# Kernel optimization log

Hardware: AMD Instinct MI355X
Metric: run time of the kernel (lower is better)

The kernel has to match this reference:

```python
import jax, jax.numpy as jnp
import numpy as np


def setup_inputs() -> dict:
    key = jax.random.key(0)
    k_x, k_q, k_k, k_v = jax.random.split(key, 4)
    B, C, H, W = 4, 256, 64, 64
    Cq = C // 4
    scale = 0.02
    x = jax.random.normal(k_x, (B, C, H, W), dtype=jnp.float32)
    Wq = jax.random.normal(k_q, (C, Cq), dtype=jnp.float32) * scale
    Wk = jax.random.normal(k_k, (C, Cq), dtype=jnp.float32) * scale
    Wv = jax.random.normal(k_v, (C, C), dtype=jnp.float32) * scale
    gamma = jnp.array([0.5], dtype=jnp.float32)
    return {"x": x, "Wq": Wq, "Wk": Wk, "Wv": Wv, "gamma": gamma}


def reference(x, Wq, Wk, Wv, gamma):
    B, C, H, W = x.shape
    N = H * W
    # [B,C,H,W] -> [B, N, C]
    xf = x.transpose(0, 2, 3, 1).reshape(B, N, C)
    q = jnp.einsum('bnc,cd->bnd', xf, Wq)   # [B, N, C//4]
    k = jnp.einsum('bnc,cd->bnd', xf, Wk)   # [B, N, C//4]
    v = jnp.einsum('bnc,cd->bnd', xf, Wv)   # [B, N, C]
    scores = jnp.einsum('bqd,bkd->bqk', q, k)        # [B, Nq, Nk]
    # NOTE: softmax over the QUERY axis (dim=1), matching the torch module.
    attn = jax.nn.softmax(scores, axis=1)
    out = gamma * jnp.einsum('bqk,bkc->bqc', attn, v) + xf   # [B, N, C]
    # [B, N, C] -> [B, C, N] -> [B, C, H, W]
    return out.transpose(0, 2, 1).reshape(B, C, H, W)
```

## Files before the change

### kernel.cpp

```cpp
#include <hip/hip_runtime.h>
#include <hip/hip_bf16.h>

#define B_ 4
#define C_ 256
#define N_ 4096
#define Dh 64

typedef __attribute__((ext_vector_type(8))) short short8;
typedef __attribute__((ext_vector_type(4))) float f32x4;


__device__ __forceinline__ ushort f2bf(float f) {
    union { float f; unsigned u; } v; v.f = f;
    unsigned u = v.u;
    return (ushort)((u + 0x7fffu + ((u >> 16) & 1u)) >> 16);
}

__device__ __forceinline__ unsigned pack2_bf16(float lo, float hi) {
    const unsigned ulo = __float_as_uint(lo) + 0x8000u;
    const unsigned uhi = __float_as_uint(hi) + 0x8000u;
    return __builtin_amdgcn_perm(uhi, ulo, 0x07060302);
}

__global__ __launch_bounds__(256) void kT(const float* __restrict__ Wq,
                                          const float* __restrict__ Wk,
                                          const float* __restrict__ Wv,
                                          ushort* __restrict__ WqT,
                                          ushort* __restrict__ WkT,
                                          ushort* __restrict__ WvT) {
    int i = blockIdx.x * 256 + threadIdx.x;
    if (i < Dh * C_) {
        int d = i / C_, c = i % C_;
        WqT[i] = f2bf(Wq[c * Dh + d]);
        WkT[i] = f2bf(Wk[c * Dh + d]);
    }
    if (i < C_ * C_) {
        int d = i / C_, c = i % C_;
        WvT[i] = f2bf(Wv[c * C_ + d]);
    }
}

__global__ __launch_bounds__(256) void kP(const float* __restrict__ x,
                                          const ushort* __restrict__ WqT,
                                          const ushort* __restrict__ WkT,
                                          const ushort* __restrict__ WvT,
                                          ushort* __restrict__ QF,
                                          ushort* __restrict__ KF,
                                          ushort* __restrict__ VF) {
    __shared__ __align__(16) ushort xT[32][264];
    const int tid = threadIdx.x;
    const int b = blockIdx.x >> 7;
    const int nbase = (blockIdx.x & 127) * 32;

    #pragma unroll
    for (int pass = 0; pass < 8; ++pass) {
        int cr = (tid >> 3) + pass * 32;
        int ns = (tid & 7) * 4;
        const f32x4 xv = *(const f32x4*)&x[(b * C_ + cr) * N_ + nbase + ns];
        #pragma unroll
        for (int j = 0; j < 4; ++j) xT[ns + j][cr] = f2bf(xv[j]);
    }
    __syncthreads();

    const int w = tid >> 6, l = tid & 63, lr = l & 15, g = l >> 4;
    f32x4 acc[2][6];
    #pragma unroll
    for (int s = 0; s < 2; ++s)
        #pragma unroll
        for (int j = 0; j < 6; ++j) acc[s][j] = (f32x4){0.f, 0.f, 0.f, 0.f};

    for (int cs = 0; cs < 8; ++cs) {
        const short8 a0 = *(const short8*)&xT[lr][cs * 32 + 8 * g];
        const short8 a1 = *(const short8*)&xT[16 + lr][cs * 32 + 8 * g];
        #pragma unroll
        for (int j = 0; j < 6; ++j) {
            const int tl = w * 6 + j;
            const ushort* src;
            if (tl < 4)      src = &WqT[(tl * 16 + lr) * C_ + cs * 32 + 8 * g];
            else if (tl < 8) src = &WkT[((tl - 4) * 16 + lr) * C_ + cs * 32 + 8 * g];
            else             src = &WvT[((tl - 8) * 16 + lr) * C_ + cs * 32 + 8 * g];
            const short8 bf = *(const short8*)src;
            acc[0][j] = __builtin_amdgcn_mfma_f32_16x16x32_bf16(a0, bf, acc[0][j], 0, 0, 0);
            acc[1][j] = __builtin_amdgcn_mfma_f32_16x16x32_bf16(a1, bf, acc[1][j], 0, 0, 0);
        }
    }

    #pragma unroll
    for (int j = 0; j < 6; ++j) {
        const int tl = w * 6 + j;
        #pragma unroll
        for (int sub = 0; sub < 2; ++sub) {
            if (tl < 8) {
                const int tlp = tl & 3;
                const int dt  = tlp >> 1;
                const int gg  = (tlp & 1) * 2 + (lr >> 3);
                const int jj  = lr & 7;
                const int rblk = (nbase >> 4) + sub;
                ushort* base = (tl < 4) ? QF : KF;
                const int bidx = (((b * 256 + rblk) * 2 + dt) * 64 + gg * 16 + 4 * g) * 8 + jj;
                #pragma unroll
                for (int r = 0; r < 4; ++r)
                    base[bidx + r * 8] = f2bf(acc[sub][j][r]);
            } else {
                const int cblk = tl - 8;
                const int kslice = nbase >> 5;
                const int gg2 = sub * 2 + (g >> 1);
                const int jj2 = 4 * (g & 1);
                ushort4 pk;
                pk.x = f2bf(acc[sub][j][0]);
                pk.y = f2bf(acc[sub][j][1]);
                pk.z = f2bf(acc[sub][j][2]);
                pk.w = f2bf(acc[sub][j][3]);
                const int vidx = (((b * 16 + cblk) * 128 + kslice) * 64 + gg2 * 16 + lr) * 8 + jj2;
                *(ushort4*)&VF[vidx] = pk;
            }
        }
    }
}

__global__ __launch_bounds__(256) void kS1(const ushort* __restrict__ QF,
                                           const ushort* __restrict__ KF,
                                           float* __restrict__ dPart) {
    const int tid = threadIdx.x;
    const int orig = blockIdx.x;
    const int b = (orig & 7) >> 1;
    const int sub = ((orig >> 3) << 1) | (orig & 1);
    const int kblk = sub & 63;
    const int qs = sub >> 6;
    const int w = tid >> 6, l = tid & 63, lr = l & 15, g = l >> 4;
    const int kcol = kblk * 64 + w * 16 + lr;

    const int krb = b * 256 + kblk * 4 + w;
    const short8 bk0 = *(const short8*)&KF[((krb * 2 + 0) * 64 + l) * 8];
    const short8 bk1 = *(const short8*)&KF[((krb * 2 + 1) * 64 + l) * 8];

    float d0 = 0.f, d1 = 0.f;
    for (int it = 0; it < 32; it += 2) {
        const int qrbA = b * 256 + qs * 32 + it;
        const short8 a0 = *(const short8*)&QF[((qrbA * 2 + 0) * 64 + l) * 8];
        const short8 a1 = *(const short8*)&QF[((qrbA * 2 + 1) * 64 + l) * 8];
        const short8 c0 = *(const short8*)&QF[(((qrbA + 1) * 2 + 0) * 64 + l) * 8];
        const short8 c1 = *(const short8*)&QF[(((qrbA + 1) * 2 + 1) * 64 + l) * 8];
        f32x4 sA = {0.f, 0.f, 0.f, 0.f}, sB = {0.f, 0.f, 0.f, 0.f};
        sA = __builtin_amdgcn_mfma_f32_16x16x32_bf16(a0, bk0, sA, 0, 0, 0);
        sA = __builtin_amdgcn_mfma_f32_16x16x32_bf16(a1, bk1, sA, 0, 0, 0);
        sB = __builtin_amdgcn_mfma_f32_16x16x32_bf16(c0, bk0, sB, 0, 0, 0);
        sB = __builtin_amdgcn_mfma_f32_16x16x32_bf16(c1, bk1, sB, 0, 0, 0);
        d0 += __expf(sA[0]) + __expf(sA[1]) + __expf(sA[2]) + __expf(sA[3]);
        d1 += __expf(sB[0]) + __expf(sB[1]) + __expf(sB[2]) + __expf(sB[3]);
    }
    float d = d0 + d1;
    #pragma unroll
    for (int off = 16; off < 64; off <<= 1)
        d += __shfl_xor(d, off, 64);
    if (l < 16)
        dPart[((b << 3) + qs) * N_ + kcol] = d;
}

__global__ __launch_bounds__(256) void kS2(const float* __restrict__ dPart,
                                           const float* __restrict__ gamma,
                                           float* __restrict__ rDArr) {
    const int i = blockIdx.x * 256 + threadIdx.x;
    const int b = i >> 12, k = i & (N_ - 1);
    float d = 0.f;
    #pragma unroll
    for (int qs = 0; qs < 8; ++qs)
        d += dPart[((b << 3) + qs) * N_ + k];
    rDArr[i] = __log2f(gamma[0] / d);
}

__global__ __launch_bounds__(512, 2) void kM(const ushort* __restrict__ QF,
                                             const ushort* __restrict__ KF,
                                             const ushort* __restrict__ VF,
                                             const float* __restrict__ rDArr,
                                             const float* __restrict__ x,
                                             float* __restrict__ out) {
    __shared__ __align__(16) ushort P[2][32][264];
    const int tid = threadIdx.x;
    const int orig = blockIdx.x;
    const int b = (orig & 7) >> 1;
    const int qblk = ((orig >> 3) << 1) | (orig & 1);
    const int qbase = qblk * 32;
    const int w = tid >> 6, l = tid & 63, lr = l & 15, g = l >> 4;

    short8 qf[2][2];
    #pragma unroll
    for (int qt = 0; qt < 2; ++qt)
        #pragma unroll
        for (int dt = 0; dt < 2; ++dt)
            qf[qt][dt] = *(const short8*)&QF[(((b * 256 + qblk * 2 + qt) * 2 + dt) * 64 + l) * 8];

    f32x4 O[2][2];
    #pragma unroll
    for (int qt = 0; qt < 2; ++qt)
        #pragma unroll
        for (int ct = 0; ct < 2; ++ct) O[qt][ct] = (f32x4){0.f, 0.f, 0.f, 0.f};

    const float* rBase = &rDArr[(size_t)b * N_];

    for (int it = 0; it < 16; ++it) {
        const int kb = it << 8;
        ushort (*Pb)[264] = P[it & 1];

        short8 vf[8][2];
        #pragma unroll
        for (int kt = 0; kt < 8; ++kt)
            #pragma unroll
            for (int ct = 0; ct < 2; ++ct)
                vf[kt][ct] = *(const short8*)&VF[(((b * 16 + w * 2 + ct) * 128 + (kb >> 5) + kt) * 64 + l) * 8];

        #pragma unroll
        for (int j = 0; j < 2; ++j) {
            const int kk0 = kb + w * 32 + j * 16;
            const int krb = b * 256 + (kk0 >> 4);
            const short8 kf0 = *(const short8*)&KF[((krb * 2 + 0) * 64 + l) * 8];
            const short8 kf1 = *(const short8*)&KF[((krb * 2 + 1) * 64 + l) * 8];
            const f32x4 rd2 = *(const f32x4*)&rBase[kk0 + 4 * g];
            const int col = (w * 32 + j * 16 + 4 * g) ^ ((lr & 12) << 1);
            #pragma unroll
            for (int qt = 0; qt < 2; ++qt) {
                f32x4 s = {0.f, 0.f, 0.f, 0.f};
                s = __builtin_amdgcn_mfma_f32_16x16x32_bf16(kf0, qf[qt][0], s, 0, 0, 0);
                s = __builtin_amdgcn_mfma_f32_16x16x32_bf16(kf1, qf[qt][1], s, 0, 0, 0);
                const float p0 = exp2f(__builtin_fmaf(s[0], 1.44269504f, rd2[0]));
                const float p1 = exp2f(__builtin_fmaf(s[1], 1.44269504f, rd2[1]));
                const float p2 = exp2f(__builtin_fmaf(s[2], 1.44269504f, rd2[2]));
                const float p3 = exp2f(__builtin_fmaf(s[3], 1.44269504f, rd2[3]));
                uint2 pk2;
                pk2.x = pack2_bf16(p0, p1);
                pk2.y = pack2_bf16(p2, p3);
                *(uint2*)&Pb[qt * 16 + lr][col] = pk2;
            }
        }
        __syncthreads();
        #pragma unroll
        for (int kt = 0; kt < 8; ++kt) {
            short8 pa[2];
            #pragma unroll
            for (int qt = 0; qt < 2; ++qt)
                pa[qt] = *(const short8*)&Pb[qt * 16 + lr][(kt * 32 + 8 * g) ^ ((lr & 12) << 1)];
            #pragma unroll
            for (int ct = 0; ct < 2; ++ct) {
                O[0][ct] = __builtin_amdgcn_mfma_f32_16x16x32_bf16(pa[0], vf[kt][ct], O[0][ct], 0, 0, 0);
                O[1][ct] = __builtin_amdgcn_mfma_f32_16x16x32_bf16(pa[1], vf[kt][ct], O[1][ct], 0, 0, 0);
            }
        }
    }

    #pragma unroll
    for (int qt = 0; qt < 2; ++qt)
        #pragma unroll
        for (int ct = 0; ct < 2; ++ct) {
            const int c = w * 32 + ct * 16 + lr;
            const int idx = (b * C_ + c) * N_ + qbase + qt * 16 + 4 * g;
            const f32x4 xr = *(const f32x4*)&x[idx];
            f32x4 o = O[qt][ct] + xr;
            *(f32x4*)&out[idx] = o;
        }
}

extern "C" void kernel_launch(void* const* d_in, const int* in_sizes, int n_in,
                              void* d_out, int out_size, void* d_ws, size_t ws_size,
                              hipStream_t stream) {
    const float* x     = (const float*)d_in[0];
    const float* Wq    = (const float*)d_in[1];
    const float* Wk    = (const float*)d_in[2];
    const float* Wv    = (const float*)d_in[3];
    const float* gamma = (const float*)d_in[4];
    float* out = (float*)d_out;

    ushort* QF  = (ushort*)d_ws;
    ushort* KF  = QF + B_ * N_ * Dh;
    ushort* VF  = KF + B_ * N_ * Dh;
    ushort* WqT = VF + B_ * C_ * N_;
    ushort* WkT = WqT + Dh * C_;
    ushort* WvT = WkT + Dh * C_;
    float*  rDArr = (float*)(WvT + C_ * C_);
    float*  dPart = rDArr + B_ * N_;

    kT<<<256, 256, 0, stream>>>(Wq, Wk, Wv, WqT, WkT, WvT);
    kP<<<512, 256, 0, stream>>>(x, WqT, WkT, WvT, QF, KF, VF);
    kS1<<<2048, 256, 0, stream>>>(QF, KF, dPart);
    kS2<<<64, 256, 0, stream>>>(dPart, gamma, rDArr);
    kM<<<512, 512, 0, stream>>>(QF, KF, VF, rDArr, x, out);
}
```

Before: 116.0 us.

## Widen main attention tile to 64 queries with 16 waves per block

Restructures the main P·V kernel so each block handles 64 queries with 1024 threads (16 waves), each wave owning 16 output channels and 16 keys per iteration instead of 32. This halves the number of blocks and the redundant K/V global reads per query, at the cost of larger LDS usage, more waves contending at each barrier, and only 256 blocks to fill the device. Launch bounds request 4 blocks per CU, which squeezes per-thread registers.

```diff
diff --git a/kernel.cpp b/kernel.cpp
--- a/kernel.cpp
+++ b/kernel.cpp
@@ -169,32 +169,31 @@
     rDArr[i] = __log2f(gamma[0] / d);
 }
 
-__global__ __launch_bounds__(512, 2) void kM(const ushort* __restrict__ QF,
-                                             const ushort* __restrict__ KF,
-                                             const ushort* __restrict__ VF,
-                                             const float* __restrict__ rDArr,
-                                             const float* __restrict__ x,
-                                             float* __restrict__ out) {
-    __shared__ __align__(16) ushort P[2][32][264];
+__global__ __launch_bounds__(1024, 4) void kM(const ushort* __restrict__ QF,
+                                              const ushort* __restrict__ KF,
+                                              const ushort* __restrict__ VF,
+                                              const float* __restrict__ rDArr,
+                                              const float* __restrict__ x,
+                                              float* __restrict__ out) {
+    __shared__ __align__(16) ushort P[2][64][264];
     const int tid = threadIdx.x;
     const int orig = blockIdx.x;
-    const int b = (orig & 7) >> 1;
-    const int qblk = ((orig >> 3) << 1) | (orig & 1);
-    const int qbase = qblk * 32;
+    const int xcd = orig & 7;
+    const int b = xcd >> 1;
+    const int qblk = ((orig >> 3) << 1) | (xcd & 1);
+    const int qbase = qblk * 64;
     const int w = tid >> 6, l = tid & 63, lr = l & 15, g = l >> 4;
 
-    short8 qf[2][2];
-    #pragma unroll
-    for (int qt = 0; qt < 2; ++qt)
+    short8 qf[4][2];
+    #pragma unroll
+    for (int qt = 0; qt < 4; ++qt)
         #pragma unroll
         for (int dt = 0; dt < 2; ++dt)
-            qf[qt][dt] = *(const short8*)&QF[(((b * 256 + qblk * 2 + qt) * 2 + dt) * 64 + l) * 8];
-
-    f32x4 O[2][2];
-    #pragma unroll
-    for (int qt = 0; qt < 2; ++qt)
-        #pragma unroll
-        for (int ct = 0; ct < 2; ++ct) O[qt][ct] = (f32x4){0.f, 0.f, 0.f, 0.f};
+            qf[qt][dt] = *(const short8*)&QF[(((b * 256 + qblk * 4 + qt) * 2 + dt) * 64 + l) * 8];
+
+    f32x4 O[4];
+    #pragma unroll
+    for (int qt = 0; qt < 4; ++qt) O[qt] = (f32x4){0.f, 0.f, 0.f, 0.f};
 
     const float* rBase = &rDArr[(size_t)b * N_];
 
@@ -202,23 +201,20 @@
         const int kb = it << 8;
         ushort (*Pb)[264] = P[it & 1];
 
-        short8 vf[8][2];
+        short8 vf[8];
         #pragma unroll
         for (int kt = 0; kt < 8; ++kt)
-            #pragma unroll
-            for (int ct = 0; ct < 2; ++ct)
-                vf[kt][ct] = *(const short8*)&VF[(((b * 16 + w * 2 + ct) * 128 + (kb >> 5) + kt) * 64 + l) * 8];
-
-        #pragma unroll
-        for (int j = 0; j < 2; ++j) {
-            const int kk0 = kb + w * 32 + j * 16;
+            vf[kt] = *(const short8*)&VF[(((b * 16 + w) * 128 + (kb >> 5) + kt) * 64 + l) * 8];
+
+        {
+            const int kk0 = kb + w * 16;
             const int krb = b * 256 + (kk0 >> 4);
             const short8 kf0 = *(const short8*)&KF[((krb * 2 + 0) * 64 + l) * 8];
             const short8 kf1 = *(const short8*)&KF[((krb * 2 + 1) * 64 + l) * 8];
             const f32x4 rd2 = *(const f32x4*)&rBase[kk0 + 4 * g];
-            const int col = (w * 32 + j * 16 + 4 * g) ^ ((lr & 12) << 1);
+            const int col = (w * 16 + 4 * g) ^ ((lr & 12) << 1);
             #pragma unroll
-            for (int qt = 0; qt < 2; ++qt) {
+            for (int qt = 0; qt < 4; ++qt) {
                 f32x4 s = {0.f, 0.f, 0.f, 0.f};
                 s = __builtin_amdgcn_mfma_f32_16x16x32_bf16(kf0, qf[qt][0], s, 0, 0, 0);
                 s = __builtin_amdgcn_mfma_f32_16x16x32_bf16(kf1, qf[qt][1], s, 0, 0, 0);
@@ -235,28 +231,22 @@
         __syncthreads();
         #pragma unroll
         for (int kt = 0; kt < 8; ++kt) {
-            short8 pa[2];
             #pragma unroll
-            for (int qt = 0; qt < 2; ++qt)
-                pa[qt] = *(const short8*)&Pb[qt * 16 + lr][(kt * 32 + 8 * g) ^ ((lr & 12) << 1)];
-            #pragma unroll
-            for (int ct = 0; ct < 2; ++ct) {
-                O[0][ct] = __builtin_amdgcn_mfma_f32_16x16x32_bf16(pa[0], vf[kt][ct], O[0][ct], 0, 0, 0);
-                O[1][ct] = __builtin_amdgcn_mfma_f32_16x16x32_bf16(pa[1], vf[kt][ct], O[1][ct], 0, 0, 0);
+            for (int qt = 0; qt < 4; ++qt) {
+                const short8 pa = *(const short8*)&Pb[qt * 16 + lr][(kt * 32 + 8 * g) ^ ((lr & 12) << 1)];
+                O[qt] = __builtin_amdgcn_mfma_f32_16x16x32_bf16(pa, vf[kt], O[qt], 0, 0, 0);
             }
         }
     }
 
     #pragma unroll
-    for (int qt = 0; qt < 2; ++qt)
-        #pragma unroll
-        for (int ct = 0; ct < 2; ++ct) {
-            const int c = w * 32 + ct * 16 + lr;
-            const int idx = (b * C_ + c) * N_ + qbase + qt * 16 + 4 * g;
-            const f32x4 xr = *(const f32x4*)&x[idx];
-            f32x4 o = O[qt][ct] + xr;
-            *(f32x4*)&out[idx] = o;
-        }
+    for (int qt = 0; qt < 4; ++qt) {
+        const int c = w * 16 + lr;
+        const int idx = (b * C_ + c) * N_ + qbase + qt * 16 + 4 * g;
+        const f32x4 xr = *(const f32x4*)&x[idx];
+        f32x4 o = O[qt] + xr;
+        *(f32x4*)&out[idx] = o;
+    }
 }
 
 extern "C" void kernel_launch(void* const* d_in, const int* in_sizes, int n_in,
@@ -282,5 +272,5 @@
     kP<<<512, 256, 0, stream>>>(x, WqT, WkT, WvT, QF, KF, VF);
     kS1<<<2048, 256, 0, stream>>>(QF, KF, dPart);
     kS2<<<64, 256, 0, stream>>>(dPart, gamma, rDArr);
-    kM<<<512, 512, 0, stream>>>(QF, KF, VF, rDArr, x, out);
-}
+    kM<<<256, 1024, 0, stream>>>(QF, KF, VF, rDArr, x, out);
+}
```

Result: faster. 107.9 us (-7.0%).
